# Kernel tuning notes

Hardware: AMD Instinct MI355X
Metric: run time of the kernel (lower is better)

The kernel has to match this reference:

```python
import jax, jax.numpy as jnp
import numpy as np

N, E = 50000, 800000
IN, HID, LAT = 512, 256, 128


def setup_inputs() -> dict:
    key = jax.random.key(0)
    ks = jax.random.split(key, 9)
    x = jax.random.normal(ks[0], (N, IN), dtype=jnp.float32)
    edge_index = jax.random.randint(ks[1], (2, E), 0, N, dtype=jnp.int64)
    edge_attr = jax.random.uniform(ks[2], (E,), dtype=jnp.float32)
    # GCNConv weights (glorot-ish scaling) and biases
    W1 = jax.random.normal(ks[3], (IN, HID), dtype=jnp.float32) / np.sqrt(IN)
    b1 = jnp.zeros((HID,), dtype=jnp.float32)
    W_mu = jax.random.normal(ks[4], (HID, LAT), dtype=jnp.float32) / np.sqrt(HID)
    b_mu = jnp.zeros((LAT,), dtype=jnp.float32)
    W_lv = jax.random.normal(ks[5], (HID, LAT), dtype=jnp.float32) / np.sqrt(HID)
    b_lv = jnp.zeros((LAT,), dtype=jnp.float32)
    return {"x": x, "edge_index": edge_index, "edge_attr": edge_attr,
            "W1": W1, "b1": b1, "W_mu": W_mu, "b_mu": b_mu,
            "W_lv": W_lv, "b_lv": b_lv}


def _gcn_norm(edge_index, edge_attr, num_nodes):
    # GCNConv default: add self-loops (weight 1), symmetric normalization
    loops = jnp.arange(num_nodes, dtype=edge_index.dtype)
    src = jnp.concatenate([edge_index[0], loops])
    dst = jnp.concatenate([edge_index[1], loops])
    w = jnp.concatenate([edge_attr, jnp.ones((num_nodes,), edge_attr.dtype)])
    deg = jax.ops.segment_sum(w, dst, num_segments=num_nodes)
    dis = jnp.where(deg > 0, jax.lax.rsqrt(jnp.maximum(deg, 1e-12)), 0.0)
    norm = dis[src] * w * dis[dst]  # [E + N]
    return src, dst, norm


def reference(x, edge_index, edge_attr, W1, b1, W_mu, b_mu, W_lv, b_lv):
    num_nodes = x.shape[0]
    src, dst, norm = _gcn_norm(edge_index, edge_attr, num_nodes)

    def conv(h, W, b):
        m = h @ W                      # dense transform [N, out]
        msg = m[src] * norm[:, None]   # gather + scale  [E+N, out]
        return jax.ops.segment_sum(msg, dst, num_segments=num_nodes) + b

    hidden = jax.nn.relu(conv(x, W1, b1))
    # Dropout(0.2) is identity in eval mode
    mu = conv(hidden, W_mu, b_mu)
    logvar = conv(hidden, W_lv, b_lv)
    return (mu, logvar)
```

## Files before the change

kernel.cpp:

```cpp
#include <hip/hip_runtime.h>

#define IN_F 512
#define HID_F 256
#define LAT_F 128

typedef __bf16 bf16x8 __attribute__((ext_vector_type(8)));
typedef float floatx4 __attribute__((ext_vector_type(4)));

__device__ __forceinline__ unsigned short f2bf(float f) {
    union { float f; unsigned u; } v; v.f = f;
    unsigned r = (v.u + 0x7fff + ((v.u >> 16) & 1)) >> 16;
    return (unsigned short)r;
}
__device__ __forceinline__ float bf2f(unsigned short h) {
    union { unsigned u; float f; } v; v.u = ((unsigned)h) << 16;
    return v.f;
}

__device__ __forceinline__ void gload_lds16(const void* g, void* lds) {
    __builtin_amdgcn_global_load_lds(
        (const __attribute__((address_space(1))) unsigned int*)(uintptr_t)g,
        (__attribute__((address_space(3))) unsigned int*)(uintptr_t)lds,
        16, 0, 0);
}


__global__ void init_nodes(float* deg, int* counts, int* fill, int N) {
    int i = blockIdx.x * 256 + threadIdx.x;
    if (i < N) { deg[i] = 1.0f; counts[i] = 1; fill[i] = 0; }
}

__global__ void edge_deg(const int* __restrict__ ei, const float* __restrict__ attr,
                         float* deg, int* counts, int E) {
    int e = blockIdx.x * 256 + threadIdx.x;
    if (e < E) {
        int d = ei[E + e];
        atomicAdd(&deg[d], attr[e]);
        atomicAdd(&counts[d], 1);
    }
}

__global__ void node_dis(const float* __restrict__ deg, float* dis, int N) {
    int i = blockIdx.x * 256 + threadIdx.x;
    if (i < N) {
        float dg = deg[i];
        dis[i] = dg > 0.f ? rsqrtf(fmaxf(dg, 1e-12f)) : 0.f;
    }
}


__global__ void scan_blocks(const int* __restrict__ counts, int* __restrict__ excl,
                            int* __restrict__ blockSums, int N) {
    __shared__ int sdata[256];
    int tid = threadIdx.x;
    int base = blockIdx.x * 1024 + tid * 4;
    int v[4]; int sum = 0;
#pragma unroll
    for (int j = 0; j < 4; ++j) { v[j] = (base + j < N) ? counts[base + j] : 0; sum += v[j]; }
    sdata[tid] = sum;
    __syncthreads();
    for (int off = 1; off < 256; off <<= 1) {
        int t = (tid >= off) ? sdata[tid - off] : 0;
        __syncthreads();
        sdata[tid] += t;
        __syncthreads();
    }
    if (tid == 255) blockSums[blockIdx.x] = sdata[255];
    int run = sdata[tid] - sum;
#pragma unroll
    for (int j = 0; j < 4; ++j) { if (base + j < N) excl[base + j] = run; run += v[j]; }
}

__global__ void scan_sums(int* blockSums, int NB) {
    __shared__ int s[64];
    int tid = threadIdx.x;
    int v = (tid < NB) ? blockSums[tid] : 0;
    s[tid] = v;
    __syncthreads();
    for (int off = 1; off < 64; off <<= 1) {
        int t = (tid >= off) ? s[tid - off] : 0;
        __syncthreads();
        s[tid] += t;
        __syncthreads();
    }
    if (tid < NB) blockSums[tid] = s[tid] - v;
}

__global__ void scan_add(int* row_ptr, const int* __restrict__ blockSums, int N, int total) {
    int tid = threadIdx.x;
    int base = blockIdx.x * 1024 + tid * 4;
    int add = blockSums[blockIdx.x];
#pragma unroll
    for (int j = 0; j < 4; ++j) if (base + j < N) row_ptr[base + j] += add;
    if (blockIdx.x == 0 && tid == 0) row_ptr[N] = total;
}


__global__ void fill_csr(const int* __restrict__ ei, const float* __restrict__ attr,
                         const float* __restrict__ dis, const int* __restrict__ row_ptr,
                         int* fill, int* col, float* val, int E, int N) {
    int e = blockIdx.x * 256 + threadIdx.x;
    if (e >= E + N) return;
    int s, d; float w;
    if (e < E) { s = ei[e]; d = ei[E + e]; w = attr[e]; }
    else       { s = d = e - E; w = 1.0f; }
    int pos = row_ptr[d] + atomicAdd(&fill[d], 1);
    col[pos] = s;
    val[pos] = dis[s] * w * dis[d];
}

__global__ void prep_w1(const float* __restrict__ W1, unsigned short* __restrict__ W1t) {
    int t = blockIdx.x * 256 + threadIdx.x;
    int n = t >> 9, k = t & 511;
    W1t[t] = f2bf(W1[(size_t)k * HID_F + n]);
}
__global__ void prep_b2(const float* __restrict__ Wmu, const float* __restrict__ Wlv,
                        unsigned short* __restrict__ B2t) {
    int t = blockIdx.x * 256 + threadIdx.x;
    int n = t >> 8, k = t & 255;
    float v = (n < 128) ? Wmu[(size_t)k * LAT_F + n] : Wlv[(size_t)k * LAT_F + (n - 128)];
    B2t[t] = f2bf(v);
}


template <bool ABF16>
__global__ __launch_bounds__(256) void gemm_mfma(const void* __restrict__ Avoid,
                                                 const unsigned short* __restrict__ Bt,
                                                 unsigned short* __restrict__ C,
                                                 int M, int K) {
    __shared__ unsigned short As[64 * 32];
    __shared__ unsigned short Bs[256 * 32];
    int tid = threadIdx.x;
    int wave = tid >> 6, lane = tid & 63;
    int mrow = lane & 15, quad = lane >> 4;
    int blockRow = blockIdx.x * 64;

    floatx4 acc[4][4];
#pragma unroll
    for (int i = 0; i < 4; ++i)
#pragma unroll
        for (int j = 0; j < 4; ++j) acc[i][j] = (floatx4){0.f, 0.f, 0.f, 0.f};

    int r = tid >> 2;
    int kq = tid & 3;
    int arow = blockRow + r; if (arow >= M) arow = M - 1;

    unsigned short* AsWaveBase = &As[wave * 512];

    for (int k0 = 0; k0 < K; k0 += 32) {
        if constexpr (ABF16) {
            const unsigned short* A = (const unsigned short*)Avoid;
            gload_lds16(A + (size_t)arow * K + k0 + kq * 8, AsWaveBase);
        } else {
            const float* A = (const float*)Avoid;
            const float* p = A + (size_t)arow * K + k0 + kq * 8;
            float4 a0 = *(const float4*)p, a1 = *(const float4*)(p + 4);
            unsigned short h[8] = {f2bf(a0.x), f2bf(a0.y), f2bf(a0.z), f2bf(a0.w),
                                   f2bf(a1.x), f2bf(a1.y), f2bf(a1.z), f2bf(a1.w)};
            *(uint4*)&As[r * 32 + kq * 8] = *(uint4*)h;
        }
#pragma unroll
        for (int pass = 0; pass < 4; ++pass) {
            int bcol = r + pass * 64;
            gload_lds16(Bt + (size_t)bcol * K + k0 + kq * 8,
                        &Bs[(pass * 256 + wave * 64) * 8]);
        }
        __syncthreads();
        bf16x8 af[4];
#pragma unroll
        for (int i = 0; i < 4; ++i)
            af[i] = *(const bf16x8*)&As[(i * 16 + mrow) * 32 + quad * 8];
#pragma unroll
        for (int j = 0; j < 4; ++j) {
            bf16x8 bf = *(const bf16x8*)&Bs[(wave * 64 + j * 16 + mrow) * 32 + quad * 8];
#pragma unroll
            for (int i = 0; i < 4; ++i)
                acc[i][j] = __builtin_amdgcn_mfma_f32_16x16x32_bf16(af[i], bf, acc[i][j], 0, 0, 0);
        }
        __syncthreads();
    }
#pragma unroll
    for (int i = 0; i < 4; ++i)
#pragma unroll
        for (int j = 0; j < 4; ++j) {
            int colo = wave * 64 + j * 16 + mrow;
#pragma unroll
            for (int v = 0; v < 4; ++v) {
                int row = blockRow + i * 16 + quad * 4 + v;
                if (row < M) C[(size_t)row * HID_F + colo] = f2bf(acc[i][j][v]);
            }
        }
}


__global__ void agg_relu(const unsigned short* __restrict__ m, const int* __restrict__ row_ptr,
                         const int* __restrict__ col, const float* __restrict__ val,
                         const float* __restrict__ bias, unsigned short* __restrict__ hidden) {
    int i = blockIdx.x, l = threadIdx.x, c0 = l << 2;
    int p0 = row_ptr[i], p1 = row_ptr[i + 1];
    float a0 = 0.f, a1 = 0.f, a2 = 0.f, a3 = 0.f;
    for (int p = p0; p < p1; ++p) {
        int s = col[p]; float w = val[p];
        ushort4 u = *(const ushort4*)(m + (size_t)s * HID_F + c0);
        a0 = fmaf(bf2f(u.x), w, a0);
        a1 = fmaf(bf2f(u.y), w, a1);
        a2 = fmaf(bf2f(u.z), w, a2);
        a3 = fmaf(bf2f(u.w), w, a3);
    }
    float4 b = *(const float4*)(bias + c0);
    a0 = fmaxf(a0 + b.x, 0.f); a1 = fmaxf(a1 + b.y, 0.f);
    a2 = fmaxf(a2 + b.z, 0.f); a3 = fmaxf(a3 + b.w, 0.f);
    ushort4 o = make_ushort4(f2bf(a0), f2bf(a1), f2bf(a2), f2bf(a3));
    *(ushort4*)(hidden + (size_t)i * HID_F + c0) = o;
}

__global__ void agg_out(const unsigned short* __restrict__ m, const int* __restrict__ row_ptr,
                        const int* __restrict__ col, const float* __restrict__ val,
                        const float* __restrict__ bmu, const float* __restrict__ blv,
                        float* __restrict__ out, int N) {
    int i = blockIdx.x, l = threadIdx.x, c0 = l << 2;
    int p0 = row_ptr[i], p1 = row_ptr[i + 1];
    float a0 = 0.f, a1 = 0.f, a2 = 0.f, a3 = 0.f;
    for (int p = p0; p < p1; ++p) {
        int s = col[p]; float w = val[p];
        ushort4 u = *(const ushort4*)(m + (size_t)s * HID_F + c0);
        a0 = fmaf(bf2f(u.x), w, a0);
        a1 = fmaf(bf2f(u.y), w, a1);
        a2 = fmaf(bf2f(u.z), w, a2);
        a3 = fmaf(bf2f(u.w), w, a3);
    }
    if (l < 32) {
        float4 b = *(const float4*)(bmu + c0);
        float4 o = make_float4(a0 + b.x, a1 + b.y, a2 + b.z, a3 + b.w);
        *(float4*)(out + (size_t)i * LAT_F + c0) = o;
    } else {
        int c = c0 - 128;
        float4 b = *(const float4*)(blv + c);
        float4 o = make_float4(a0 + b.x, a1 + b.y, a2 + b.z, a3 + b.w);
        *(float4*)(out + (size_t)(N + i) * LAT_F + c) = o;
    }
}


extern "C" void kernel_launch(void* const* d_in, const int* in_sizes, int n_in,
                              void* d_out, int out_size, void* d_ws, size_t ws_size,
                              hipStream_t stream) {
    const float* x    = (const float*)d_in[0];
    const int*   ei   = (const int*)d_in[1];
    const float* attr = (const float*)d_in[2];
    const float* W1   = (const float*)d_in[3];
    const float* b1   = (const float*)d_in[4];
    const float* Wmu  = (const float*)d_in[5];
    const float* bmu  = (const float*)d_in[6];
    const float* Wlv  = (const float*)d_in[7];
    const float* blv  = (const float*)d_in[8];
    float* out = (float*)d_out;

    const int N  = in_sizes[0] / IN_F;
    const int E  = in_sizes[2];
    const int EN = E + N;

    char* w = (char*)d_ws;
    size_t off = 0;
    auto carve = [&](size_t bytes) -> void* {
        void* p = w + off; off += (bytes + 255) & ~(size_t)255; return p;
    };
    float*          deg       = (float*)carve((size_t)N * 4);
    float*          dis       = (float*)carve((size_t)N * 4);
    int*            counts    = (int*)  carve((size_t)N * 4);
    int*            fill      = (int*)  carve((size_t)N * 4);
    int*            row_ptr   = (int*)  carve((size_t)(N + 1) * 4);
    int*            blockSums = (int*)  carve(64 * 4);
    int*            col       = (int*)  carve((size_t)EN * 4);
    float*          val       = (float*)carve((size_t)EN * 4);
    unsigned short* W1t       = (unsigned short*)carve((size_t)HID_F * IN_F * 2);
    unsigned short* B2t       = (unsigned short*)carve((size_t)HID_F * HID_F * 2);
    unsigned short* m         = (unsigned short*)carve((size_t)N * HID_F * 2);
    unsigned short* hidden    = (unsigned short*)carve((size_t)N * HID_F * 2);

    int nb256 = (N + 255) / 256;
    init_nodes<<<nb256, 256, 0, stream>>>(deg, counts, fill, N);
    edge_deg<<<(E + 255) / 256, 256, 0, stream>>>(ei, attr, deg, counts, E);
    node_dis<<<nb256, 256, 0, stream>>>(deg, dis, N);

    int NB = (N + 1023) / 1024;
    scan_blocks<<<NB, 256, 0, stream>>>(counts, row_ptr, blockSums, N);
    scan_sums<<<1, 64, 0, stream>>>(blockSums, NB);
    scan_add<<<NB, 256, 0, stream>>>(row_ptr, blockSums, N, EN);

    fill_csr<<<(EN + 255) / 256, 256, 0, stream>>>(ei, attr, dis, row_ptr, fill, col, val, E, N);

    prep_w1<<<(HID_F * IN_F + 255) / 256, 256, 0, stream>>>(W1, W1t);
    prep_b2<<<(HID_F * HID_F + 255) / 256, 256, 0, stream>>>(Wmu, Wlv, B2t);

    int gblocks = (N + 63) / 64;
    gemm_mfma<false><<<gblocks, 256, 0, stream>>>(x, W1t, m, N, IN_F);
    agg_relu<<<N, 64, 0, stream>>>(m, row_ptr, col, val, b1, hidden);
    gemm_mfma<true><<<gblocks, 256, 0, stream>>>(hidden, B2t, m, N, HID_F);
    agg_out<<<N, 64, 0, stream>>>(m, row_ptr, col, val, bmu, blv, out, N);
}
```

Measured before the change: 502.0 us.

## Pack degree and count into one 64-bit fixed-point atomic and reuse slot positions

Degree weight and edge count are now accumulated together in a single 64-bit atomicAdd, with the edge weight held as fixed point scaled by 2^20. The old count returned by that atomic becomes the edge's slot in its CSR row, which removes the second atomic pass in fill_csr and the fill array. The init, W1 transpose and B2 transpose kernels are merged into one launch. This trades float precision for fixed-point degree sums, adds an E-sized slot buffer, and relies on the low 32 bits not overflowing into the count.

```diff
diff --git a/kernel.cpp b/kernel.cpp
--- a/kernel.cpp
+++ b/kernel.cpp
@@ -6,6 +6,8 @@
 
 typedef __bf16 bf16x8 __attribute__((ext_vector_type(8)));
 typedef float floatx4 __attribute__((ext_vector_type(4)));
+
+#define FIX_SCALE 1048576.0f
 
 __device__ __forceinline__ unsigned short f2bf(float f) {
     union { float f; unsigned u; } v; v.f = f;
@@ -25,25 +27,42 @@
 }
 
 
-__global__ void init_nodes(float* deg, int* counts, int* fill, int N) {
-    int i = blockIdx.x * 256 + threadIdx.x;
-    if (i < N) { deg[i] = 1.0f; counts[i] = 1; fill[i] = 0; }
-}
+__global__ void prep_all(const float* __restrict__ W1, const float* __restrict__ Wmu,
+                         const float* __restrict__ Wlv, unsigned long long* __restrict__ packed,
+                         unsigned short* __restrict__ W1t, unsigned short* __restrict__ B2t,
+                         int N) {
+    int t = blockIdx.x * 256 + threadIdx.x;
+    if (t < N) packed[t] = (1ULL << 32) | (unsigned long long)(unsigned)FIX_SCALE;
+    if (t < HID_F * IN_F) {
+        int n = t >> 9, k = t & 511;
+        W1t[t] = f2bf(W1[(size_t)k * HID_F + n]);
+    }
+    if (t < HID_F * HID_F) {
+        int n = t >> 8, k = t & 255;
+        float v = (n < 128) ? Wmu[(size_t)k * LAT_F + n] : Wlv[(size_t)k * LAT_F + (n - 128)];
+        B2t[t] = f2bf(v);
+    }
+}
+
 
 __global__ void edge_deg(const int* __restrict__ ei, const float* __restrict__ attr,
-                         float* deg, int* counts, int E) {
+                         unsigned long long* __restrict__ packed, int* __restrict__ slot, int E) {
     int e = blockIdx.x * 256 + threadIdx.x;
     if (e < E) {
         int d = ei[E + e];
-        atomicAdd(&deg[d], attr[e]);
-        atomicAdd(&counts[d], 1);
-    }
-}
-
-__global__ void node_dis(const float* __restrict__ deg, float* dis, int N) {
+        unsigned fw = __float2uint_rn(attr[e] * FIX_SCALE);
+        unsigned long long old = atomicAdd(&packed[d], (1ULL << 32) | (unsigned long long)fw);
+        slot[e] = (int)(old >> 32);
+    }
+}
+
+__global__ void node_dis(const unsigned long long* __restrict__ packed,
+                         float* __restrict__ dis, int* __restrict__ counts, int N) {
     int i = blockIdx.x * 256 + threadIdx.x;
     if (i < N) {
-        float dg = deg[i];
+        unsigned long long p = packed[i];
+        counts[i] = (int)(p >> 32);
+        float dg = (float)(unsigned)(p & 0xffffffffu) * (1.0f / FIX_SCALE);
         dis[i] = dg > 0.f ? rsqrtf(fmaxf(dg, 1e-12f)) : 0.f;
     }
 }
@@ -97,29 +116,17 @@
 
 
 __global__ void fill_csr(const int* __restrict__ ei, const float* __restrict__ attr,
-                         const float* __restrict__ dis, const int* __restrict__ row_ptr,
-                         int* fill, int* col, float* val, int E, int N) {
+                         const int* __restrict__ slot, const float* __restrict__ dis,
+                         const int* __restrict__ row_ptr,
+                         int* __restrict__ col, float* __restrict__ val, int E, int N) {
     int e = blockIdx.x * 256 + threadIdx.x;
     if (e >= E + N) return;
-    int s, d; float w;
-    if (e < E) { s = ei[e]; d = ei[E + e]; w = attr[e]; }
-    else       { s = d = e - E; w = 1.0f; }
-    int pos = row_ptr[d] + atomicAdd(&fill[d], 1);
+    int s, d, sl; float w;
+    if (e < E) { s = ei[e]; d = ei[E + e]; w = attr[e]; sl = slot[e]; }
+    else       { s = d = e - E; w = 1.0f; sl = 0; }
+    int pos = row_ptr[d] + sl;
     col[pos] = s;
     val[pos] = dis[s] * w * dis[d];
-}
-
-__global__ void prep_w1(const float* __restrict__ W1, unsigned short* __restrict__ W1t) {
-    int t = blockIdx.x * 256 + threadIdx.x;
-    int n = t >> 9, k = t & 511;
-    W1t[t] = f2bf(W1[(size_t)k * HID_F + n]);
-}
-__global__ void prep_b2(const float* __restrict__ Wmu, const float* __restrict__ Wlv,
-                        unsigned short* __restrict__ B2t) {
-    int t = blockIdx.x * 256 + threadIdx.x;
-    int n = t >> 8, k = t & 255;
-    float v = (n < 128) ? Wmu[(size_t)k * LAT_F + n] : Wlv[(size_t)k * LAT_F + (n - 128)];
-    B2t[t] = f2bf(v);
 }
 
 
@@ -265,12 +272,12 @@
     auto carve = [&](size_t bytes) -> void* {
         void* p = w + off; off += (bytes + 255) & ~(size_t)255; return p;
     };
-    float*          deg       = (float*)carve((size_t)N * 4);
+    unsigned long long* packed = (unsigned long long*)carve((size_t)N * 8);
     float*          dis       = (float*)carve((size_t)N * 4);
     int*            counts    = (int*)  carve((size_t)N * 4);
-    int*            fill      = (int*)  carve((size_t)N * 4);
     int*            row_ptr   = (int*)  carve((size_t)(N + 1) * 4);
     int*            blockSums = (int*)  carve(64 * 4);
+    int*            slot      = (int*)  carve((size_t)E * 4);
     int*            col       = (int*)  carve((size_t)EN * 4);
     float*          val       = (float*)carve((size_t)EN * 4);
     unsigned short* W1t       = (unsigned short*)carve((size_t)HID_F * IN_F * 2);
@@ -278,20 +285,17 @@
     unsigned short* m         = (unsigned short*)carve((size_t)N * HID_F * 2);
     unsigned short* hidden    = (unsigned short*)carve((size_t)N * HID_F * 2);
 
-    int nb256 = (N + 255) / 256;
-    init_nodes<<<nb256, 256, 0, stream>>>(deg, counts, fill, N);
-    edge_deg<<<(E + 255) / 256, 256, 0, stream>>>(ei, attr, deg, counts, E);
-    node_dis<<<nb256, 256, 0, stream>>>(deg, dis, N);
+    prep_all<<<(HID_F * IN_F + 255) / 256, 256, 0, stream>>>(W1, Wmu, Wlv, packed, W1t, B2t, N);
+
+    edge_deg<<<(E + 255) / 256, 256, 0, stream>>>(ei, attr, packed, slot, E);
+    node_dis<<<(N + 255) / 256, 256, 0, stream>>>(packed, dis, counts, N);
 
     int NB = (N + 1023) / 1024;
     scan_blocks<<<NB, 256, 0, stream>>>(counts, row_ptr, blockSums, N);
     scan_sums<<<1, 64, 0, stream>>>(blockSums, NB);
     scan_add<<<NB, 256, 0, stream>>>(row_ptr, blockSums, N, EN);
 
-    fill_csr<<<(EN + 255) / 256, 256, 0, stream>>>(ei, attr, dis, row_ptr, fill, col, val, E, N);
-
-    prep_w1<<<(HID_F * IN_F + 255) / 256, 256, 0, stream>>>(W1, W1t);
-    prep_b2<<<(HID_F * HID_F + 255) / 256, 256, 0, stream>>>(Wmu, Wlv, B2t);
+    fill_csr<<<(EN + 255) / 256, 256, 0, stream>>>(ei, attr, slot, dis, row_ptr, col, val, E, N);
 
     int gblocks = (N + 63) / 64;
     gemm_mfma<false><<<gblocks, 256, 0, stream>>>(x, W1t, m, N, IN_F);
```

Result: faster. 440.0 us (-12.3%).
